# Performance work log

Hardware: AMD Instinct MI355X
Metric: run time of the kernel (lower is better)

Reference implementation:

```python
import jax, jax.numpy as jnp
import numpy as np

# --- model dims (from init args) ---
LAYERS = 6
LEAF = 2 ** (LAYERS - 1)        # 32
M_LEN = 128
CAM_NUM = 2
MAIN_CAM = 0
LATENT = 48
H_LAT = 2048                    # LatentNet hidden
H_BR = 512                      # ChooseBranchNet hidden
B = 16384

# Path bits: for leaf i, bit at classifier depth d (root->leaf order) is
# (i >> (LAYERS-2-d)) & 1. This is exactly what the search_table + double
# advanced-indexing gather in the torch code computes (heap tree routing).
_BITS = ((np.arange(LEAF)[:, None] >> np.arange(LAYERS - 2, -1, -1)[None, :]) & 1)  # [LEAF, LAYERS-1]
BITS = jnp.asarray(_BITS, dtype=jnp.int32)


def setup_inputs() -> dict:
    key = jax.random.key(0)
    ks = jax.random.split(key, 9)
    s = lambda fan: 1.0 / np.sqrt(fan)
    return {
        "batch_data": jax.random.normal(ks[0], (B, CAM_NUM, M_LEN), dtype=jnp.float32),
        # LatentNet: [B, 2*M_LEN] -> hidden -> LEAF*LATENT
        "Wl1": jax.random.normal(ks[1], (2 * M_LEN, H_LAT), dtype=jnp.float32) * s(2 * M_LEN),
        "bl1": jnp.zeros((H_LAT,), dtype=jnp.float32),
        "Wl2": jax.random.normal(ks[2], (H_LAT, LEAF * LATENT), dtype=jnp.float32) * s(H_LAT),
        "bl2": jnp.zeros((LEAF * LATENT,), dtype=jnp.float32),
        # ChooseBranchNet (shared across the LAYERS-1 classifier slots): M_LEN -> hidden -> 2
        "Wb1": jax.random.normal(ks[3], (M_LEN, H_BR), dtype=jnp.float32) * s(M_LEN),
        "bb1": jnp.zeros((H_BR,), dtype=jnp.float32),
        "Wb2": jax.random.normal(ks[4], (H_BR, 2), dtype=jnp.float32) * s(H_BR),
        "bb2": jnp.zeros((2,), dtype=jnp.float32),
    }


def reference(batch_data, Wl1, bl1, Wl2, bl2, Wb1, bb1, Wb2, bb2):
    bsz = batch_data.shape[0]
    # expand_measurements: main cam repeated (LAYERS-1) times -> [B, LAYERS-1, M_LEN]
    main = batch_data[:, MAIN_CAM]                                  # [B, M_LEN]
    x_br = jnp.broadcast_to(main[:, None, :], (bsz, LAYERS - 1, M_LEN))
    # ChooseBranchNet -> per-layer 2-way probabilities
    h = jax.nn.relu(jnp.einsum('blm,mh->blh', x_br, Wb1) + bb1)
    p = jax.nn.softmax(jnp.einsum('blh,ho->blo', h, Wb2) + bb2, axis=-1)  # [B, L-1, 2]
    # Tree gates: product of path-branch probabilities along root->leaf path.
    comp = jnp.where(BITS[None] == 1, p[:, None, :, 1], p[:, None, :, 0])  # [B, LEAF, L-1]
    gates = jnp.prod(comp, axis=-1)                                        # [B, LEAF]
    # top-1 routing (argsort(...)[:, -1] as in the torch code)
    router = jnp.argsort(gates, axis=-1)[:, -1]                            # [B]
    # LatentNet on concatenated two-camera measurements
    x2 = jnp.concatenate([batch_data[:, 0], batch_data[:, 1]], axis=-1)    # [B, 2*M_LEN]
    hl = jax.nn.relu(x2 @ Wl1 + bl1)
    nn_latent = (hl @ Wl2 + bl2).reshape(bsz, LEAF, LATENT)
    # scatter-select per-sample leaf latent (replaces the torch.where loop)
    select = jnp.take_along_axis(nn_latent, router[:, None, None], axis=1)[:, 0]  # [B, LATENT]
    return select
```

## Files before the change

### kernel.cpp

```cpp
#include <hip/hip_runtime.h>
#include <stdint.h>

typedef short bf16x8 __attribute__((ext_vector_type(8)));
typedef float f32x4 __attribute__((ext_vector_type(4)));

#define NROWS 16384
#define K1DIM 256
#define N1DIM 2048
#define N2DIM 96

#define GLD16(g, l) __builtin_amdgcn_global_load_lds( \
    (const __attribute__((address_space(1))) uint32_t*)(g), \
    (__attribute__((address_space(3))) uint32_t*)(l), 16, 0, 0)

__device__ __forceinline__ ushort f2bf(float x) {
  union { float f; uint32_t u; } c; c.f = x;
  uint32_t u = c.u;
  return (ushort)((u + 0x7FFFu + ((u >> 16) & 1u)) >> 16);
}

__global__ __launch_bounds__(256) void k0_convert(
    const float* __restrict__ bd, const float* __restrict__ Wl1,
    const float* __restrict__ Wl2, ushort* __restrict__ x2bf,
    ushort* __restrict__ wl1t, ushort* __restrict__ w2t) {
  int i = blockIdx.x * 256 + threadIdx.x;
  if (i < NROWS * 256) x2bf[i] = f2bf(bd[i]);
  if (i < 2048 * 256) {
    int n = i >> 8, k = i & 255;
    wl1t[i] = f2bf(Wl1[k * 2048 + n]);
  }
  if (i < 96 * 2048) {
    int j = i >> 11, k = i & 2047;
    int col = (j < 48) ? j : (1440 + j);
    w2t[i] = f2bf(Wl2[k * 1536 + col]);
  }
}

__global__ __launch_bounds__(256) void k1_branch(
    const float* __restrict__ bd, const float* __restrict__ Wb1,
    const float* __restrict__ Wb2, const float* __restrict__ bb1,
    const float* __restrict__ bb2, int* __restrict__ router) {
  __shared__ __align__(16) float xs[128 * 64];
  __shared__ __align__(16) float wsh[128 * 64];
  const int t = threadIdx.x;
  const int ln = t & 63, wv = t >> 6;
  const int rb = blockIdx.x * 64;

  {
    int r = t & 63, c0 = t >> 6;
#pragma unroll
    for (int p = 0; p < 8; p++) {
      int c = c0 + p * 4;
      float4 v = *(const float4*)(bd + (size_t)(rb + r) * 256 + c * 4);
      xs[(c * 4 + 0) * 64 + r] = v.x;
      xs[(c * 4 + 1) * 64 + r] = v.y;
      xs[(c * 4 + 2) * 64 + r] = v.z;
      xs[(c * 4 + 3) * 64 + r] = v.w;
    }
  }

  const int jj = ln & 31;
  const int rowbase = (wv << 4) + ((ln >> 5) << 3);
  float score[8];
#pragma unroll
  for (int i = 0; i < 8; i++) score[i] = 0.f;

  for (int jc = 0; jc < 8; jc++) {
    int j0 = jc * 64;
    __syncthreads();
    {
      int q4 = (t & 15) * 4;
      int mb = t >> 4;
#pragma unroll
      for (int p = 0; p < 8; p++) {
        int m = mb + p * 16;
        float4 v = *(const float4*)(Wb1 + (size_t)m * 512 + j0 + q4);
        *(float4*)(&wsh[m * 64 + q4]) = v;
      }
    }
    __syncthreads();

    float b1A = bb1[j0 + jj];
    float b1B = bb1[j0 + 32 + jj];
    float aA[8], aB[8];
#pragma unroll
    for (int i = 0; i < 8; i++) { aA[i] = b1A; aB[i] = b1B; }

#pragma unroll 4
    for (int m = 0; m < 128; m++) {
      float wA = wsh[(m << 6) + jj];
      float wB = wsh[(m << 6) + 32 + jj];
      const float* xp = &xs[(m << 6) + rowbase];
      float4 x0 = *(const float4*)(xp);
      float4 x1 = *(const float4*)(xp + 4);
      float xv[8] = {x0.x, x0.y, x0.z, x0.w, x1.x, x1.y, x1.z, x1.w};
#pragma unroll
      for (int i = 0; i < 8; i++) {
        aA[i] = fmaf(wA, xv[i], aA[i]);
        aB[i] = fmaf(wB, xv[i], aB[i]);
      }
    }
    int jA = j0 + jj, jB = jA + 32;
    float wdA = Wb2[jA * 2 + 1] - Wb2[jA * 2];
    float wdB = Wb2[jB * 2 + 1] - Wb2[jB * 2];
#pragma unroll
    for (int i = 0; i < 8; i++)
      score[i] += fmaxf(aA[i], 0.f) * wdA + fmaxf(aB[i], 0.f) * wdB;
  }

#pragma unroll
  for (int off = 1; off <= 16; off <<= 1) {
#pragma unroll
    for (int i = 0; i < 8; i++) score[i] += __shfl_xor(score[i], off);
  }
  float c = bb2[1] - bb2[0];
  if ((ln & 31) == 0) {
    int rbase = rb + rowbase;
#pragma unroll
    for (int i = 0; i < 8; i++)
      router[rbase + i] = (score[i] + c >= 0.f) ? 1 : 0;
  }
}

__global__ __launch_bounds__(256) void k2_gemm1(
    const ushort* __restrict__ A, const ushort* __restrict__ BT,
    const float* __restrict__ bl1, ushort* __restrict__ hl) {
  __shared__ __align__(1024) ushort As[128 * 64];
  __shared__ __align__(1024) ushort Bs[128 * 64];
  const int t = threadIdx.x, ln = t & 63, wv = t >> 6;
  const int m0 = blockIdx.y << 7;
  const int n0 = blockIdx.x << 7;
  const int wm = (wv >> 1) << 6, wn = (wv & 1) << 6;
  const int rsub = ln >> 3, kc8 = ln & 7;
  const int q = ln >> 4, rr = ln & 15;

  f32x4 acc[4][4] = {};

  for (int k0 = 0; k0 < K1DIM; k0 += 64) {
#pragma unroll
    for (int i = 0; i < 4; i++) {
      int inst = (wv << 2) + i;
      int row = (inst << 3) + rsub;
      GLD16(A + (size_t)(m0 + row) * K1DIM + k0 + (kc8 << 3), As + (inst << 9));
      GLD16(BT + (size_t)(n0 + row) * K1DIM + k0 + (kc8 << 3), Bs + (inst << 9));
    }
    __syncthreads();
#pragma unroll
    for (int kk = 0; kk < 2; kk++) {
      int kb = ((kk << 2) + q) << 3;
      bf16x8 af[4], bfr[4];
#pragma unroll
      for (int mi = 0; mi < 4; mi++)
        af[mi] = *(const bf16x8*)(As + (((wm + (mi << 4) + rr)) << 6) + kb);
#pragma unroll
      for (int ni = 0; ni < 4; ni++)
        bfr[ni] = *(const bf16x8*)(Bs + (((wn + (ni << 4) + rr)) << 6) + kb);
#pragma unroll
      for (int mi = 0; mi < 4; mi++)
#pragma unroll
        for (int ni = 0; ni < 4; ni++)
          acc[mi][ni] = __builtin_amdgcn_mfma_f32_16x16x32_bf16(
              af[mi], bfr[ni], acc[mi][ni], 0, 0, 0);
    }
    __syncthreads();
  }

#pragma unroll
  for (int ni = 0; ni < 4; ni++) {
    int col = n0 + wn + (ni << 4) + rr;
    float bias = bl1[col];
#pragma unroll
    for (int mi = 0; mi < 4; mi++) {
      int rowb = m0 + wm + (mi << 4) + (q << 2);
      f32x4 a = acc[mi][ni];
#pragma unroll
      for (int v = 0; v < 4; v++) {
        float val = fmaxf(a[v] + bias, 0.f);
        hl[(size_t)(rowb + v) * N1DIM + col] = f2bf(val);
      }
    }
  }
}

__global__ __launch_bounds__(256) void k2b_gemm2(
    const ushort* __restrict__ hl, const ushort* __restrict__ w2t,
    float* __restrict__ P) {
  __shared__ __align__(1024) ushort As[64 * 64];
  __shared__ __align__(1024) ushort Bs[96 * 64];
  const int t = threadIdx.x, ln = t & 63, wv = t >> 6;
  const int ks = blockIdx.x;
  const int rb = blockIdx.y << 6;
  const int rsub = ln >> 3, kc8 = ln & 7;
  const int q = ln >> 4, rr = ln & 15;
  float* Pout = P + (size_t)ks * NROWS * N2DIM;
  const int kbase = ks << 10;

  f32x4 acc[6] = {};

  for (int k0 = 0; k0 < 1024; k0 += 64) {
    int kg = kbase + k0;
#pragma unroll
    for (int i = 0; i < 2; i++) {
      int inst = (wv << 1) + i;
      int row = (inst << 3) + rsub;
      GLD16(hl + (size_t)(rb + row) * N1DIM + kg + (kc8 << 3), As + (inst << 9));
    }
#pragma unroll
    for (int i = 0; i < 3; i++) {
      int inst = wv * 3 + i;
      int row = (inst << 3) + rsub;
      GLD16(w2t + (size_t)row * N1DIM + kg + (kc8 << 3), Bs + (inst << 9));
    }
    __syncthreads();
#pragma unroll
    for (int kk = 0; kk < 2; kk++) {
      int kb = ((kk << 2) + q) << 3;
      bf16x8 af = *(const bf16x8*)(As + (((wv << 4) + rr) << 6) + kb);
#pragma unroll
      for (int ni = 0; ni < 6; ni++) {
        bf16x8 bfr = *(const bf16x8*)(Bs + (((ni << 4) + rr) << 6) + kb);
        acc[ni] = __builtin_amdgcn_mfma_f32_16x16x32_bf16(af, bfr, acc[ni], 0, 0, 0);
      }
    }
    __syncthreads();
  }

#pragma unroll
  for (int ni = 0; ni < 6; ni++) {
#pragma unroll
    for (int v = 0; v < 4; v++) {
      int row = rb + (wv << 4) + (q << 2) + v;
      int col = (ni << 4) + rr;
      Pout[(size_t)row * N2DIM + col] = acc[ni][v];
    }
  }
}

__global__ __launch_bounds__(256) void k3_select(
    const float* __restrict__ P0, const float* __restrict__ P1,
    const float* __restrict__ bl2, const int* __restrict__ router,
    float* __restrict__ out) {
  int t = blockIdx.x * 256 + threadIdx.x;
  int b = t / 12, i4 = (t % 12) * 4;
  int sel = router[b];
  int cb = sel ? 48 : 0;
  int bb = sel ? 1488 : 0;
  float4 p0 = *(const float4*)(P0 + (size_t)b * N2DIM + cb + i4);
  float4 p1 = *(const float4*)(P1 + (size_t)b * N2DIM + cb + i4);
  float4 bz = *(const float4*)(bl2 + bb + i4);
  float4 r;
  r.x = p0.x + p1.x + bz.x;
  r.y = p0.y + p1.y + bz.y;
  r.z = p0.z + p1.z + bz.z;
  r.w = p0.w + p1.w + bz.w;
  *(float4*)(out + (size_t)b * 48 + i4) = r;
}

extern "C" void kernel_launch(void* const* d_in, const int* in_sizes, int n_in,
                              void* d_out, int out_size, void* d_ws, size_t ws_size,
                              hipStream_t stream) {
  const float* bd  = (const float*)d_in[0];
  const float* Wl1 = (const float*)d_in[1];
  const float* bl1 = (const float*)d_in[2];
  const float* Wl2 = (const float*)d_in[3];
  const float* bl2 = (const float*)d_in[4];
  const float* Wb1 = (const float*)d_in[5];
  const float* bb1 = (const float*)d_in[6];
  const float* Wb2 = (const float*)d_in[7];
  const float* bb2 = (const float*)d_in[8];

  char* ws = (char*)d_ws;
  ushort* x2bf  = (ushort*)(ws);
  ushort* wl1t  = (ushort*)(ws + 8388608);
  ushort* w2t   = (ushort*)(ws + 9437184);
  ushort* hl    = (ushort*)(ws + 9830400);
  float*  P     = (float*)(ws + 76939264);
  int*    router= (int*)(ws + 89522176);
  float*  outp  = (float*)d_out;

  k0_convert<<<dim3(16384), dim3(256), 0, stream>>>(bd, Wl1, Wl2, x2bf, wl1t, w2t);
  k1_branch<<<dim3(256), dim3(256), 0, stream>>>(bd, Wb1, Wb2, bb1, bb2, router);
  k2_gemm1<<<dim3(16, 128), dim3(256), 0, stream>>>(x2bf, wl1t, bl1, hl);
  k2b_gemm2<<<dim3(2, 256), dim3(256), 0, stream>>>(hl, w2t, P);
  k3_select<<<dim3(768), dim3(256), 0, stream>>>(P, P + (size_t)NROWS * N2DIM, bl2,
                                                 router, outp);
}
```

Before: 190.5 us.

## Compute branch scores with bf16 MFMA and recheck near-margin rows in fp32

Replaces the fp32 scalar branch-score kernel with a bf16 MFMA GEMM that writes partial scores, a classify kernel that sets router bits and collects rows whose score lies within a fixed margin of zero, and a recheck kernel that recomputes those rows in fp32. The aim is to move the branch MLP onto matrix cores and cut the fp32 FMA cost. It adds a Wb1 transpose in the convert kernel, a memset, an atomic counter and two extra launches. Correctness depends on the fixed 0.03 margin covering the bf16 rounding error.

```diff
diff --git a/kernel.cpp b/kernel.cpp
--- a/kernel.cpp
+++ b/kernel.cpp
@@ -8,6 +8,7 @@
 #define K1DIM 256
 #define N1DIM 2048
 #define N2DIM 96
+#define MARGIN 0.03f
 
 #define GLD16(g, l) __builtin_amdgcn_global_load_lds( \
     (const __attribute__((address_space(1))) uint32_t*)(g), \
@@ -21,8 +22,9 @@
 
 __global__ __launch_bounds__(256) void k0_convert(
     const float* __restrict__ bd, const float* __restrict__ Wl1,
-    const float* __restrict__ Wl2, ushort* __restrict__ x2bf,
-    ushort* __restrict__ wl1t, ushort* __restrict__ w2t) {
+    const float* __restrict__ Wl2, const float* __restrict__ Wb1,
+    ushort* __restrict__ x2bf, ushort* __restrict__ wl1t,
+    ushort* __restrict__ w2t, ushort* __restrict__ wb1t) {
   int i = blockIdx.x * 256 + threadIdx.x;
   if (i < NROWS * 256) x2bf[i] = f2bf(bd[i]);
   if (i < 2048 * 256) {
@@ -34,91 +36,156 @@
     int col = (j < 48) ? j : (1440 + j);
     w2t[i] = f2bf(Wl2[k * 1536 + col]);
   }
-}
-
-__global__ __launch_bounds__(256) void k1_branch(
+  if (i < 512 * 128) {
+    int j = i >> 7, m = i & 127;
+    wb1t[i] = f2bf(Wb1[m * 512 + j]);
+  }
+}
+
+__global__ __launch_bounds__(256) void k1a_score(
+    const ushort* __restrict__ x2bf, const ushort* __restrict__ wb1t,
+    const float* __restrict__ bb1, const float* __restrict__ Wb2,
+    float* __restrict__ part) {
+  __shared__ __align__(1024) ushort As[128 * 64];
+  __shared__ __align__(1024) ushort Bs[128 * 64];
+  const int t = threadIdx.x, ln = t & 63, wv = t >> 6;
+  const int m0 = blockIdx.y << 7;
+  const int n0 = blockIdx.x << 7;
+  const int wm = (wv >> 1) << 6, wn = (wv & 1) << 6;
+  const int rsub = ln >> 3, kc8 = ln & 7;
+  const int q = ln >> 4, rr = ln & 15;
+
+  f32x4 acc[4][4] = {};
+
+  for (int k0 = 0; k0 < 128; k0 += 64) {
+#pragma unroll
+    for (int i = 0; i < 4; i++) {
+      int inst = (wv << 2) + i;
+      int row = (inst << 3) + rsub;
+      GLD16(x2bf + (size_t)(m0 + row) * 256 + k0 + (kc8 << 3), As + (inst << 9));
+      GLD16(wb1t + (size_t)(n0 + row) * 128 + k0 + (kc8 << 3), Bs + (inst << 9));
+    }
+    __syncthreads();
+#pragma unroll
+    for (int kk = 0; kk < 2; kk++) {
+      int kb = ((kk << 2) + q) << 3;
+      bf16x8 af[4], bfr[4];
+#pragma unroll
+      for (int mi = 0; mi < 4; mi++)
+        af[mi] = *(const bf16x8*)(As + (((wm + (mi << 4) + rr)) << 6) + kb);
+#pragma unroll
+      for (int ni = 0; ni < 4; ni++)
+        bfr[ni] = *(const bf16x8*)(Bs + (((wn + (ni << 4) + rr)) << 6) + kb);
+#pragma unroll
+      for (int mi = 0; mi < 4; mi++)
+#pragma unroll
+        for (int ni = 0; ni < 4; ni++)
+          acc[mi][ni] = __builtin_amdgcn_mfma_f32_16x16x32_bf16(
+              af[mi], bfr[ni], acc[mi][ni], 0, 0, 0);
+    }
+    __syncthreads();
+  }
+
+  float s4[4][4] = {};
+#pragma unroll
+  for (int ni = 0; ni < 4; ni++) {
+    int col = n0 + wn + (ni << 4) + rr;
+    float bias = bb1[col];
+    float wdv = Wb2[col * 2 + 1] - Wb2[col * 2];
+#pragma unroll
+    for (int mi = 0; mi < 4; mi++) {
+      f32x4 a = acc[mi][ni];
+#pragma unroll
+      for (int v = 0; v < 4; v++)
+        s4[mi][v] += fmaxf(a[v] + bias, 0.f) * wdv;
+    }
+  }
+#pragma unroll
+  for (int off = 1; off <= 8; off <<= 1)
+#pragma unroll
+    for (int mi = 0; mi < 4; mi++)
+#pragma unroll
+      for (int v = 0; v < 4; v++)
+        s4[mi][v] += __shfl_xor(s4[mi][v], off);
+
+  if (rr == 0) {
+    float* dst = part + (size_t)(blockIdx.x * 2 + (wv & 1)) * NROWS +
+                 m0 + wm + (q << 2);
+#pragma unroll
+    for (int mi = 0; mi < 4; mi++) {
+      float4 v4 = make_float4(s4[mi][0], s4[mi][1], s4[mi][2], s4[mi][3]);
+      *(float4*)(dst + (mi << 4)) = v4;
+    }
+  }
+}
+
+__global__ __launch_bounds__(256) void k1b_classify(
+    const float* __restrict__ part, const float* __restrict__ bb2,
+    int* __restrict__ router, int* __restrict__ list, int* __restrict__ counter) {
+  int t = blockIdx.x * 256 + threadIdx.x;
+  float s = bb2[1] - bb2[0];
+#pragma unroll
+  for (int i = 0; i < 8; i++) s += part[i * NROWS + t];
+  router[t] = (s >= 0.f) ? 1 : 0;
+  if (fabsf(s) < MARGIN) {
+    int idx = atomicAdd(counter, 1);
+    list[idx] = t;
+  }
+}
+
+__global__ __launch_bounds__(256) void k1c_recheck(
     const float* __restrict__ bd, const float* __restrict__ Wb1,
     const float* __restrict__ Wb2, const float* __restrict__ bb1,
-    const float* __restrict__ bb2, int* __restrict__ router) {
-  __shared__ __align__(16) float xs[128 * 64];
-  __shared__ __align__(16) float wsh[128 * 64];
-  const int t = threadIdx.x;
-  const int ln = t & 63, wv = t >> 6;
-  const int rb = blockIdx.x * 64;
-
-  {
-    int r = t & 63, c0 = t >> 6;
-#pragma unroll
-    for (int p = 0; p < 8; p++) {
-      int c = c0 + p * 4;
-      float4 v = *(const float4*)(bd + (size_t)(rb + r) * 256 + c * 4);
-      xs[(c * 4 + 0) * 64 + r] = v.x;
-      xs[(c * 4 + 1) * 64 + r] = v.y;
-      xs[(c * 4 + 2) * 64 + r] = v.z;
-      xs[(c * 4 + 3) * 64 + r] = v.w;
-    }
-  }
-
-  const int jj = ln & 31;
-  const int rowbase = (wv << 4) + ((ln >> 5) << 3);
-  float score[8];
-#pragma unroll
-  for (int i = 0; i < 8; i++) score[i] = 0.f;
-
-  for (int jc = 0; jc < 8; jc++) {
-    int j0 = jc * 64;
-    __syncthreads();
-    {
-      int q4 = (t & 15) * 4;
-      int mb = t >> 4;
-#pragma unroll
-      for (int p = 0; p < 8; p++) {
-        int m = mb + p * 16;
-        float4 v = *(const float4*)(Wb1 + (size_t)m * 512 + j0 + q4);
-        *(float4*)(&wsh[m * 64 + q4]) = v;
+    const float* __restrict__ bb2, const int* __restrict__ list,
+    const int* __restrict__ counter, int* __restrict__ router) {
+  const int ln = threadIdx.x & 63;
+  const int wid = (blockIdx.x * 256 + threadIdx.x) >> 6;
+  const int count = *counter;
+  const float c = bb2[1] - bb2[0];
+
+  for (int base = wid * 4; base < count; base += 512 * 4) {
+    int rows[4];
+#pragma unroll
+    for (int r = 0; r < 4; r++) {
+      int idx = base + r;
+      rows[r] = list[(idx < count) ? idx : base];
+    }
+    float acc[4][8];
+#pragma unroll
+    for (int r = 0; r < 4; r++)
+#pragma unroll
+      for (int u = 0; u < 8; u++) acc[r][u] = 0.f;
+
+    for (int m = 0; m < 128; m++) {
+      float w[8];
+#pragma unroll
+      for (int u = 0; u < 8; u++) w[u] = Wb1[m * 512 + (u << 6) + ln];
+#pragma unroll
+      for (int r = 0; r < 4; r++) {
+        float x = bd[(size_t)rows[r] * 256 + m];
+#pragma unroll
+        for (int u = 0; u < 8; u++) acc[r][u] = fmaf(x, w[u], acc[r][u]);
       }
     }
-    __syncthreads();
-
-    float b1A = bb1[j0 + jj];
-    float b1B = bb1[j0 + 32 + jj];
-    float aA[8], aB[8];
-#pragma unroll
-    for (int i = 0; i < 8; i++) { aA[i] = b1A; aB[i] = b1B; }
-
-#pragma unroll 4
-    for (int m = 0; m < 128; m++) {
-      float wA = wsh[(m << 6) + jj];
-      float wB = wsh[(m << 6) + 32 + jj];
-      const float* xp = &xs[(m << 6) + rowbase];
-      float4 x0 = *(const float4*)(xp);
-      float4 x1 = *(const float4*)(xp + 4);
-      float xv[8] = {x0.x, x0.y, x0.z, x0.w, x1.x, x1.y, x1.z, x1.w};
-#pragma unroll
-      for (int i = 0; i < 8; i++) {
-        aA[i] = fmaf(wA, xv[i], aA[i]);
-        aB[i] = fmaf(wB, xv[i], aB[i]);
+    float sc[4];
+#pragma unroll
+    for (int r = 0; r < 4; r++) {
+      float s = 0.f;
+#pragma unroll
+      for (int u = 0; u < 8; u++) {
+        int j = (u << 6) + ln;
+        float wd = Wb2[j * 2 + 1] - Wb2[j * 2];
+        s += fmaxf(acc[r][u] + bb1[j], 0.f) * wd;
       }
-    }
-    int jA = j0 + jj, jB = jA + 32;
-    float wdA = Wb2[jA * 2 + 1] - Wb2[jA * 2];
-    float wdB = Wb2[jB * 2 + 1] - Wb2[jB * 2];
-#pragma unroll
-    for (int i = 0; i < 8; i++)
-      score[i] += fmaxf(aA[i], 0.f) * wdA + fmaxf(aB[i], 0.f) * wdB;
-  }
-
-#pragma unroll
-  for (int off = 1; off <= 16; off <<= 1) {
-#pragma unroll
-    for (int i = 0; i < 8; i++) score[i] += __shfl_xor(score[i], off);
-  }
-  float c = bb2[1] - bb2[0];
-  if ((ln & 31) == 0) {
-    int rbase = rb + rowbase;
-#pragma unroll
-    for (int i = 0; i < 8; i++)
-      router[rbase + i] = (score[i] + c >= 0.f) ? 1 : 0;
+#pragma unroll
+      for (int off = 1; off <= 32; off <<= 1) s += __shfl_xor(s, off);
+      sc[r] = s + c;
+    }
+    if (ln == 0) {
+#pragma unroll
+      for (int r = 0; r < 4; r++)
+        if (base + r < count) router[rows[r]] = (sc[r] >= 0.f) ? 1 : 0;
+    }
   }
 }
 
@@ -276,10 +343,19 @@
   ushort* hl    = (ushort*)(ws + 9830400);
   float*  P     = (float*)(ws + 76939264);
   int*    router= (int*)(ws + 89522176);
+  ushort* wb1t  = (ushort*)(ws + 89587712);
+  float*  part  = (float*)(ws + 89718784);
+  int*    list  = (int*)(ws + 90243072);
+  int*    counter=(int*)(ws + 90308608);
   float*  outp  = (float*)d_out;
 
-  k0_convert<<<dim3(16384), dim3(256), 0, stream>>>(bd, Wl1, Wl2, x2bf, wl1t, w2t);
-  k1_branch<<<dim3(256), dim3(256), 0, stream>>>(bd, Wb1, Wb2, bb1, bb2, router);
+  k0_convert<<<dim3(16384), dim3(256), 0, stream>>>(bd, Wl1, Wl2, Wb1,
+                                                    x2bf, wl1t, w2t, wb1t);
+  hipMemsetAsync(counter, 0, 4, stream);
+  k1a_score<<<dim3(4, 128), dim3(256), 0, stream>>>(x2bf, wb1t, bb1, Wb2, part);
+  k1b_classify<<<dim3(64), dim3(256), 0, stream>>>(part, bb2, router, list, counter);
+  k1c_recheck<<<dim3(128), dim3(256), 0, stream>>>(bd, Wb1, Wb2, bb1, bb2,
+                                                   list, counter, router);
   k2_gemm1<<<dim3(16, 128), dim3(256), 0, stream>>>(x2bf, wl1t, bl1, hl);
   k2b_gemm2<<<dim3(2, 256), dim3(256), 0, stream>>>(hl, w2t, P);
   k3_select<<<dim3(768), dim3(256), 0, stream>>>(P, P + (size_t)NROWS * N2DIM, bl2,
```

Result: faster. 184.2 us (-3.3%).
